# Performance work log

Hardware: AMD Instinct MI355X
Metric: run time of the kernel (lower is better)

## Reference

```python
import jax, jax.numpy as jnp
import numpy as np
from jax import lax

N = 1_000_000
H = 1024
POOL = 8
NF = 16
NS = 50
K = 5
PAD = (K - 1) // 2
D_IN = 3 + NF + NS  # 69
EPS = 1e-4


def setup_inputs() -> dict:
    key = jax.random.key(0)
    ks = jax.random.split(key, 14)
    def dense(k, fan_in, fan_out):
        lim = 1.0 / np.sqrt(fan_in)
        kw, kb = jax.random.split(k)
        w = jax.random.uniform(kw, (fan_in, fan_out), jnp.float32, -lim, lim)
        b = jax.random.uniform(kb, (fan_out,), jnp.float32, -lim, lim)
        return w, b
    x = jax.random.uniform(ks[0], (N, 2), jnp.float32)
    s = jax.random.normal(ks[1], (N, 1), jnp.float32)
    sse = jax.random.normal(ks[2], (N, NS), jnp.float32)
    sdf = jax.random.normal(ks[3], (1, 2, H, H), jnp.float32)
    lim_c = 1.0 / np.sqrt(2 * K * K)
    conv_w = jax.random.uniform(ks[4], (NF, 2, K, K), jnp.float32, -lim_c, lim_c)
    conv_b = jax.random.uniform(ks[5], (NF,), jnp.float32, -lim_c, lim_c)
    w1, b1 = dense(ks[6], D_IN, 128)
    w2, b2 = dense(ks[7], 128, 128)
    w3, b3 = dense(ks[8], 128, 96)
    w4, b4 = dense(ks[9], 96, 1)
    return {"x": x, "s": s, "sse": sse, "sdf": sdf,
            "conv_w": conv_w, "conv_b": conv_b,
            "w1": w1, "b1": b1, "w2": w2, "b2": b2,
            "w3": w3, "b3": b3, "w4": w4, "b4": b4}


def tensor_interp2d(A, pts, dx):
    # A: [C, Hh, Ww] feature map; pts: [N, 2] coords in [0,1] -> returns [N, C]
    C, Hh, Ww = A.shape
    gx = jnp.clip(pts[:, 0], dx, 1.0 - dx) * (Ww - 1)
    gy = jnp.clip(pts[:, 1], dx, 1.0 - dx) * (Hh - 1)
    x0 = jnp.floor(gx).astype(jnp.int32)
    y0 = jnp.floor(gy).astype(jnp.int32)
    x1 = jnp.minimum(x0 + 1, Ww - 1)
    y1 = jnp.minimum(y0 + 1, Hh - 1)
    wx = (gx - x0)[None, :]  # [1, N]
    wy = (gy - y0)[None, :]
    f00 = A[:, y0, x0]  # [C, N]
    f10 = A[:, y0, x1]
    f01 = A[:, y1, x0]
    f11 = A[:, y1, x1]
    out = (f00 * (1 - wx) * (1 - wy) + f10 * wx * (1 - wy)
           + f01 * (1 - wx) * wy + f11 * wx * wy)
    return out.T  # [N, C]


def reference(x, s, sse, sdf, conv_w, conv_b, w1, b1, w2, b2, w3, b3, w4, b4):
    # AvgPool2d(8, stride=8): exact reshape-mean since stride == kernel
    B, Cin, Hh, Ww = sdf.shape
    pooled = sdf.reshape(B, Cin, Hh // POOL, POOL, Ww // POOL, POOL).mean(axis=(3, 5))
    feat = lax.conv_general_dilated(pooled, conv_w, (1, 1), [(PAD, PAD), (PAD, PAD)],
                                    dimension_numbers=("NCHW", "OIHW", "NCHW"))
    feat = feat + conv_b[None, :, None, None]
    A = feat[0]  # squeeze -> [NF, 128, 128]
    x1 = tensor_interp2d(A, x, EPS)  # [N, NF]
    h = jnp.concatenate((x, s, sse, x1), axis=1)  # [N, 69]
    h = jax.nn.relu(h @ w1 + b1)
    h = jax.nn.relu(h @ w2 + b2)
    h = jax.nn.relu(h @ w3 + b3)
    return h @ w4 + b4  # [N, 1]
```

## Files before the change

kernel.cpp:

```cpp
#include <hip/hip_runtime.h>

#define EPS_ 1e-4f

typedef _Float16 f16;
typedef _Float16 f16x8 __attribute__((ext_vector_type(8)));
typedef _Float16 f16x4 __attribute__((ext_vector_type(4)));
typedef _Float16 f16x2 __attribute__((ext_vector_type(2)));
typedef __fp16 h16x2 __attribute__((ext_vector_type(2)));
typedef float f32x4v __attribute__((ext_vector_type(4)));
typedef float f32x2v __attribute__((ext_vector_type(2)));
typedef unsigned int u32;

__device__ inline f32x4v mfma16(f16x8 a, f16x8 b, f32x4v c) {
    return __builtin_amdgcn_mfma_f32_16x16x32_f16(a, b, c, 0, 0, 0);
}
__device__ inline f16x2 pk2(float a, float b) {
    h16x2 r = __builtin_amdgcn_cvt_pkrtz(a, b);
    return __builtin_bit_cast(f16x2, r);
}
__device__ inline u32 bc32(f16x2 v) { return __builtin_bit_cast(u32, v); }

__device__ inline f16x8 zero8() {
    f16x8 r;
#pragma unroll
    for (int i = 0; i < 8; i++) r[i] = (f16)0.f;
    return r;
}

__device__ inline f16x8 cvt8x2(f32x2v a, f32x2v b, f32x2v c, f32x2v d) {
    f16x2 p0 = pk2(a.x, a.y), p1 = pk2(b.x, b.y), p2 = pk2(c.x, c.y), p3 = pk2(d.x, d.y);
    f16x8 r;
    r[0] = p0[0]; r[1] = p0[1]; r[2] = p1[0]; r[3] = p1[1];
    r[4] = p2[0]; r[5] = p2[1]; r[6] = p3[0]; r[7] = p3[1];
    return r;
}

__global__ void pool_kernel(const float* __restrict__ sdf, float* __restrict__ pooled) {
    int t = blockIdx.x * blockDim.x + threadIdx.x;
    int c = t >> 14;
    int rem = t & 16383;
    int R = rem >> 7;
    int C = rem & 127;
    const float* base = sdf + c * 1048576 + (R * 8) * 1024 + C * 8;
    float sum = 0.f;
#pragma unroll
    for (int r = 0; r < 8; r++) {
        const float4* p = (const float4*)(base + r * 1024);
        float4 a = p[0];
        float4 b = p[1];
        sum += a.x + a.y + a.z + a.w + b.x + b.y + b.z + b.w;
    }
    pooled[t] = sum * (1.f / 64.f);
}

__global__ void conv_kernel(const float* __restrict__ pooled,
                            const float* __restrict__ conv_w,
                            const float* __restrict__ conv_b,
                            float* __restrict__ A) {
    int t = blockIdx.x * blockDim.x + threadIdx.x;
    int y = t >> 7, x = t & 127;
    float acc[16];
#pragma unroll
    for (int f = 0; f < 16; f++) acc[f] = conv_b[f];
#pragma unroll
    for (int c = 0; c < 2; c++) {
#pragma unroll
        for (int ky = 0; ky < 5; ky++) {
            int yy = y + ky - 2;
            if (yy < 0 || yy > 127) continue;
#pragma unroll
            for (int kx = 0; kx < 5; kx++) {
                int xx = x + kx - 2;
                if (xx < 0 || xx > 127) continue;
                float v = pooled[c * 16384 + yy * 128 + xx];
                int wbase = c * 25 + ky * 5 + kx;
#pragma unroll
                for (int f = 0; f < 16; f++)
                    acc[f] = fmaf(v, conv_w[f * 50 + wbase], acc[f]);
            }
        }
    }
    float4* out4 = (float4*)(A + t * 16);
#pragma unroll
    for (int q = 0; q < 4; q++)
        out4[q] = make_float4(acc[4 * q], acc[4 * q + 1], acc[4 * q + 2], acc[4 * q + 3]);
}

__global__ void pack_kernel(const float* __restrict__ w1, const float* __restrict__ b1,
                            const float* __restrict__ w2, const float* __restrict__ w3,
                            f16* __restrict__ frags) {
    int t = blockIdx.x * blockDim.x + threadIdx.x;
    if (t >= 80 * 64) return;
    int f = t >> 6, lane = t & 63;
    int g = lane >> 4, col = lane & 15;
    f16 v[8];
    if (f < 24) {
        int mf = f / 3, kc = f % 3;
        int o = mf * 16 + col;
#pragma unroll
        for (int i = 0; i < 8; i++) {
            int k = kc * 32 + g * 8 + i;
            float val = 0.f;
            if (k < 50) val = w1[(3 + k) * 128 + o];
            else if (k == 50) val = w1[0 * 128 + o];
            else if (k == 51) val = w1[1 * 128 + o];
            else if (k == 52) val = w1[2 * 128 + o];
            else if (k >= 56 && k < 72) val = w1[(53 + (k - 56)) * 128 + o];
            else if (k == 72) val = b1[o];
            v[i] = (f16)val;
        }
    } else if (f < 56) {
        int ff = f - 24, mf = ff >> 2, kc = ff & 3;
        int o = mf * 16 + col;
#pragma unroll
        for (int i = 0; i < 8; i++) {
            int k = kc * 32 + g * 8 + i;
            v[i] = (f16)w2[k * 128 + o];
        }
    } else {
        int ff = f - 56, mf = ff >> 2, kc = ff & 3;
        int o = mf * 16 + col;
#pragma unroll
        for (int i = 0; i < 8; i++) {
            int k = kc * 32 + g * 8 + i;
            v[i] = (f16)w3[k * 96 + o];
        }
    }
    f16* dst = frags + (f * 64 + lane) * 8;
#pragma unroll
    for (int i = 0; i < 8; i++) dst[i] = v[i];
}

__global__ void __launch_bounds__(512, 2) mlp_kernel(
    const float* __restrict__ x, const float* __restrict__ s,
    const float* __restrict__ sse, const float* __restrict__ Amat,
    const float4* __restrict__ fragsv,
    const float* __restrict__ b2, const float* __restrict__ b3,
    const float* __restrict__ w4, const float* __restrict__ b4,
    float* __restrict__ out) {
    __shared__ f16 wlds[40960];
    __shared__ f16 acth[8][2048];
    __shared__ u32 ibuf[8][2][192];
    __shared__ float bias2[128];
    __shared__ float bias3[96];
    __shared__ float w4l[96];

    const int tid = threadIdx.x;
    const int wv = tid >> 6;
    const int lane = tid & 63;
    const int g = lane >> 4, col = lane & 15;
    const int swz = (col & 7) << 3;

    {
        float4* wl4 = (float4*)wlds;
        for (int i = tid; i < 5120; i += 512) wl4[i] = fragsv[i];
        for (int i = tid; i < 128; i += 512) bias2[i] = b2[i];
        for (int i = tid; i < 96; i += 512) { bias3[i] = b3[i]; w4l[i] = w4[i]; }
    }
    __syncthreads();
    const float b4v = b4[0];

    f16* ah = acth[wv];
    u32* ibA = ibuf[wv][0];
    u32* ibB = ibuf[wv][1];

    const int wtotal = 31250;
    int wg = blockIdx.x * 8 + wv;
    const int wstride = gridDim.x * 8;

    f32x2v Ac0[4], Ac1[4], Ae, Axv; float Asv;
    f32x2v Bc0[4], Bc1[4], Be, Bxv; float Bsv;

    auto LOADT = [&](int pt0, f32x2v* c0, f32x2v* c1, f32x2v& e, f32x2v& xv, float& sv) {
        const float* base = sse + (long)(pt0 + col) * 50;
#pragma unroll
        for (int q = 0; q < 4; q++) c0[q] = *(const f32x2v*)(base + 8 * g + 2 * q);
        if (g < 2) {
#pragma unroll
            for (int q = 0; q < 4; q++) c1[q] = *(const f32x2v*)(base + 32 + 8 * g + 2 * q);
        } else if (g == 2) {
            e = *(const f32x2v*)(base + 48);
            sv = s[pt0 + col];
        }
        xv = *(const f32x2v*)(x + 2 * (pt0 + col));
    };

    auto INTERP = [&](f32x2v xv, u32* ib) {
        float gx = fminf(fmaxf(xv.x, EPS_), 1.f - EPS_) * 127.f;
        float gy = fminf(fmaxf(xv.y, EPS_), 1.f - EPS_) * 127.f;
        float fx0 = floorf(gx), fy0 = floorf(gy);
        int ix0 = (int)fx0, iy0 = (int)fy0;
        int ix1 = min(ix0 + 1, 127), iy1 = min(iy0 + 1, 127);
        float wx = gx - fx0, wy = gy - fy0;
        const f32x4v* A4 = (const f32x4v*)Amat;
        f32x4v f00 = A4[(iy0 * 128 + ix0) * 4 + g];
        f32x4v f10 = A4[(iy0 * 128 + ix1) * 4 + g];
        f32x4v f01 = A4[(iy1 * 128 + ix0) * 4 + g];
        f32x4v f11 = A4[(iy1 * 128 + ix1) * 4 + g];
        float w00 = (1.f - wx) * (1.f - wy), w10 = wx * (1.f - wy);
        float w01 = (1.f - wx) * wy, w11 = wx * wy;
        f32x4v r = f00 * w00 + f10 * w10 + f01 * w01 + f11 * w11;
        uint2 uv;
        uv.x = bc32(pk2(r.x, r.y));
        uv.y = bc32(pk2(r.z, r.w));
        *(uint2*)(ib + col * 12 + 2 * g) = uv;
    };

    auto BUILD = [&](f32x2v* c0, f32x2v* c1, f32x2v e, f32x2v xv, float sv,
                     const u32* ib, f16x8* bf) {
        bf[0] = cvt8x2(c0[0], c0[1], c0[2], c0[3]);
        if (g < 2) {
            bf[1] = cvt8x2(c1[0], c1[1], c1[2], c1[3]);
        } else if (g == 2) {
            f16x8 t = zero8();
            t[0] = (f16)e.x; t[1] = (f16)e.y;
            t[2] = (f16)xv.x; t[3] = (f16)xv.y;
            t[4] = (f16)sv;
            bf[1] = t;
        } else {
            bf[1] = *(const f16x8*)(ib + col * 12);
        }
        if (g == 0) {
            bf[2] = *(const f16x8*)(ib + col * 12 + 4);
        } else if (g == 1) {
            f16x8 t = zero8();
            t[0] = (f16)1.f;
            bf[2] = t;
        } else {
            bf[2] = zero8();
        }
    };

    auto TRANS = [&](f32x4v* acc, const float* bias, f16x8* hbf) {
#pragma unroll
        for (int mf = 0; mf < 8; mf++) {
            f32x4v v = acc[mf];
            if (bias) {
                f32x4v bb = *(const f32x4v*)&bias[mf * 16 + g * 4];
                v = v + bb;
            }
            uint2 uv;
            uv.x = bc32(pk2(fmaxf(v.x, 0.f), fmaxf(v.y, 0.f)));
            uv.y = bc32(pk2(fmaxf(v.z, 0.f), fmaxf(v.w, 0.f)));
            *(uint2*)&ah[(col * 128 + mf * 16 + g * 4) ^ swz] = uv;
        }
#pragma unroll
        for (int kc = 0; kc < 4; kc++)
            hbf[kc] = *(const f16x8*)&ah[(col * 128 + kc * 32 + g * 8) ^ swz];
    };

    auto L4OUT = [&](f32x4v* acc3, int pt0) {
        float partial = 0.f;
#pragma unroll
        for (int mf = 0; mf < 6; mf++) {
            f32x4v bb = *(const f32x4v*)&bias3[mf * 16 + g * 4];
            f32x4v wv4 = *(const f32x4v*)&w4l[mf * 16 + g * 4];
            partial += fmaxf(acc3[mf].x + bb.x, 0.f) * wv4.x;
            partial += fmaxf(acc3[mf].y + bb.y, 0.f) * wv4.y;
            partial += fmaxf(acc3[mf].z + bb.z, 0.f) * wv4.z;
            partial += fmaxf(acc3[mf].w + bb.w, 0.f) * wv4.w;
        }
        partial += __shfl_xor(partial, 16);
        partial += __shfl_xor(partial, 32);
        if (g == 0) out[pt0 + col] = partial + b4v;
    };

    if (wg < wtotal) {
        LOADT(wg * 32, Ac0, Ac1, Ae, Axv, Asv);
        LOADT(wg * 32 + 16, Bc0, Bc1, Be, Bxv, Bsv);
    }

    for (; wg < wtotal; wg += wstride) {
        const int pt0 = wg * 32;

        INTERP(Axv, ibA);
        INTERP(Bxv, ibB);

        f16x8 bfA[3], bfB[3];
        BUILD(Ac0, Ac1, Ae, Axv, Asv, ibA, bfA);
        BUILD(Bc0, Bc1, Be, Bxv, Bsv, ibB, bfB);

        int wgn = wg + wstride;
        if (wgn < wtotal) {
            LOADT(wgn * 32, Ac0, Ac1, Ae, Axv, Asv);
            LOADT(wgn * 32 + 16, Bc0, Bc1, Be, Bxv, Bsv);
        }

        f32x4v accA[8], accB[8];
#pragma unroll
        for (int mf = 0; mf < 8; mf++) {
            accA[mf] = (f32x4v)(0.f);
            accB[mf] = (f32x4v)(0.f);
        }
#pragma unroll
        for (int kc = 0; kc < 3; kc++) {
#pragma unroll
            for (int mf = 0; mf < 8; mf++) {
                f16x8 wf = *(const f16x8*)&wlds[((mf * 3 + kc) * 64 + lane) * 8];
                accA[mf] = mfma16(wf, bfA[kc], accA[mf]);
                accB[mf] = mfma16(wf, bfB[kc], accB[mf]);
            }
        }

        f16x8 hbfA[4], hbfB[4];
        TRANS(accA, nullptr, hbfA);
        TRANS(accB, nullptr, hbfB);

        f32x4v acc2A[8], acc2B[8];
#pragma unroll
        for (int mf = 0; mf < 8; mf++) {
            acc2A[mf] = (f32x4v)(0.f);
            acc2B[mf] = (f32x4v)(0.f);
        }
#pragma unroll
        for (int kc = 0; kc < 4; kc++) {
#pragma unroll
            for (int mf = 0; mf < 8; mf++) {
                f16x8 wf = *(const f16x8*)&wlds[((24 + mf * 4 + kc) * 64 + lane) * 8];
                acc2A[mf] = mfma16(wf, hbfA[kc], acc2A[mf]);
                acc2B[mf] = mfma16(wf, hbfB[kc], acc2B[mf]);
            }
        }

        TRANS(acc2A, bias2, hbfA);
        TRANS(acc2B, bias2, hbfB);

        f32x4v acc3A[6], acc3B[6];
#pragma unroll
        for (int mf = 0; mf < 6; mf++) {
            acc3A[mf] = (f32x4v)(0.f);
            acc3B[mf] = (f32x4v)(0.f);
        }
#pragma unroll
        for (int kc = 0; kc < 4; kc++) {
#pragma unroll
            for (int mf = 0; mf < 6; mf++) {
                f16x8 wf = *(const f16x8*)&wlds[((56 + mf * 4 + kc) * 64 + lane) * 8];
                acc3A[mf] = mfma16(wf, hbfA[kc], acc3A[mf]);
                acc3B[mf] = mfma16(wf, hbfB[kc], acc3B[mf]);
            }
        }

        L4OUT(acc3A, pt0);
        L4OUT(acc3B, pt0 + 16);
    }
}

extern "C" void kernel_launch(void* const* d_in, const int* in_sizes, int n_in,
                              void* d_out, int out_size, void* d_ws, size_t ws_size,
                              hipStream_t stream) {
    const float* x      = (const float*)d_in[0];
    const float* s      = (const float*)d_in[1];
    const float* sse    = (const float*)d_in[2];
    const float* sdf    = (const float*)d_in[3];
    const float* conv_w = (const float*)d_in[4];
    const float* conv_b = (const float*)d_in[5];
    const float* w1     = (const float*)d_in[6];
    const float* b1     = (const float*)d_in[7];
    const float* w2     = (const float*)d_in[8];
    const float* b2     = (const float*)d_in[9];
    const float* w3     = (const float*)d_in[10];
    const float* b3     = (const float*)d_in[11];
    const float* w4     = (const float*)d_in[12];
    const float* b4     = (const float*)d_in[13];
    float* out = (float*)d_out;

    float* pooled = (float*)d_ws;
    float* A      = pooled + 32768;
    f16*   frags  = (f16*)d_ws;

    pool_kernel<<<128, 256, 0, stream>>>(sdf, pooled);
    conv_kernel<<<64, 256, 0, stream>>>(pooled, conv_w, conv_b, A);
    pack_kernel<<<20, 256, 0, stream>>>(w1, b1, w2, w3, frags);
    mlp_kernel<<<256, 512, 0, stream>>>(x, s, sse, A, (const float4*)frags,
                                        b2, b3, w4, b4, out);
}
```

Measured before the change: 132.3 us.

## Process four 16-point tiles per wave to amortize LDS weight fragment loads

Each wave now handles 64 points per iteration (four tiles) instead of 32, so every weight fragment read from LDS feeds four MFMAs instead of two. The prefetch of the next iteration's inputs also moves from right after BUILD to after layer 3, which shortens the window it has to hide global latency. Register pressure roughly doubles (four sets of accumulators and prefetched inputs) under launch_bounds(512,2), which risks spills or lower occupancy.

```diff
diff --git a/kernel.cpp b/kernel.cpp
--- a/kernel.cpp
+++ b/kernel.cpp
@@ -140,7 +140,7 @@
     float* __restrict__ out) {
     __shared__ f16 wlds[40960];
     __shared__ f16 acth[8][2048];
-    __shared__ u32 ibuf[8][2][192];
+    __shared__ u32 ibuf[8][4][192];
     __shared__ float bias2[128];
     __shared__ float bias3[96];
     __shared__ float w4l[96];
@@ -161,33 +161,32 @@
     const float b4v = b4[0];
 
     f16* ah = acth[wv];
-    u32* ibA = ibuf[wv][0];
-    u32* ibB = ibuf[wv][1];
-
-    const int wtotal = 31250;
+
+    const int wtotal = 15625;
     int wg = blockIdx.x * 8 + wv;
     const int wstride = gridDim.x * 8;
 
-    f32x2v Ac0[4], Ac1[4], Ae, Axv; float Asv;
-    f32x2v Bc0[4], Bc1[4], Be, Bxv; float Bsv;
-
-    auto LOADT = [&](int pt0, f32x2v* c0, f32x2v* c1, f32x2v& e, f32x2v& xv, float& sv) {
+    f32x2v c0[4][4], c1[4][4], e4[4], xv4[4];
+    float sv4[4];
+
+    auto LOADT = [&](int pt0, int t) {
         const float* base = sse + (long)(pt0 + col) * 50;
 #pragma unroll
-        for (int q = 0; q < 4; q++) c0[q] = *(const f32x2v*)(base + 8 * g + 2 * q);
+        for (int q = 0; q < 4; q++) c0[t][q] = *(const f32x2v*)(base + 8 * g + 2 * q);
         if (g < 2) {
 #pragma unroll
-            for (int q = 0; q < 4; q++) c1[q] = *(const f32x2v*)(base + 32 + 8 * g + 2 * q);
+            for (int q = 0; q < 4; q++) c1[t][q] = *(const f32x2v*)(base + 32 + 8 * g + 2 * q);
         } else if (g == 2) {
-            e = *(const f32x2v*)(base + 48);
-            sv = s[pt0 + col];
-        }
-        xv = *(const f32x2v*)(x + 2 * (pt0 + col));
-    };
-
-    auto INTERP = [&](f32x2v xv, u32* ib) {
-        float gx = fminf(fmaxf(xv.x, EPS_), 1.f - EPS_) * 127.f;
-        float gy = fminf(fmaxf(xv.y, EPS_), 1.f - EPS_) * 127.f;
+            e4[t] = *(const f32x2v*)(base + 48);
+            sv4[t] = s[pt0 + col];
+        }
+        xv4[t] = *(const f32x2v*)(x + 2 * (pt0 + col));
+    };
+
+    auto INTERP = [&](int t) {
+        f32x2v xvv = xv4[t];
+        float gx = fminf(fmaxf(xvv.x, EPS_), 1.f - EPS_) * 127.f;
+        float gy = fminf(fmaxf(xvv.y, EPS_), 1.f - EPS_) * 127.f;
         float fx0 = floorf(gx), fy0 = floorf(gy);
         int ix0 = (int)fx0, iy0 = (int)fy0;
         int ix1 = min(ix0 + 1, 127), iy1 = min(iy0 + 1, 127);
@@ -203,35 +202,34 @@
         uint2 uv;
         uv.x = bc32(pk2(r.x, r.y));
         uv.y = bc32(pk2(r.z, r.w));
-        *(uint2*)(ib + col * 12 + 2 * g) = uv;
-    };
-
-    auto BUILD = [&](f32x2v* c0, f32x2v* c1, f32x2v e, f32x2v xv, float sv,
-                     const u32* ib, f16x8* bf) {
-        bf[0] = cvt8x2(c0[0], c0[1], c0[2], c0[3]);
+        *(uint2*)(&ibuf[wv][t][0] + col * 12 + 2 * g) = uv;
+    };
+
+    auto BUILD = [&](int t, f16x8* bf) {
+        bf[0] = cvt8x2(c0[t][0], c0[t][1], c0[t][2], c0[t][3]);
         if (g < 2) {
-            bf[1] = cvt8x2(c1[0], c1[1], c1[2], c1[3]);
+            bf[1] = cvt8x2(c1[t][0], c1[t][1], c1[t][2], c1[t][3]);
         } else if (g == 2) {
-            f16x8 t = zero8();
-            t[0] = (f16)e.x; t[1] = (f16)e.y;
-            t[2] = (f16)xv.x; t[3] = (f16)xv.y;
-            t[4] = (f16)sv;
-            bf[1] = t;
+            f16x8 tt = zero8();
+            tt[0] = (f16)e4[t].x; tt[1] = (f16)e4[t].y;
+            tt[2] = (f16)xv4[t].x; tt[3] = (f16)xv4[t].y;
+            tt[4] = (f16)sv4[t];
+            bf[1] = tt;
         } else {
-            bf[1] = *(const f16x8*)(ib + col * 12);
+            bf[1] = *(const f16x8*)(&ibuf[wv][t][0] + col * 12);
         }
         if (g == 0) {
-            bf[2] = *(const f16x8*)(ib + col * 12 + 4);
+            bf[2] = *(const f16x8*)(&ibuf[wv][t][0] + col * 12 + 4);
         } else if (g == 1) {
-            f16x8 t = zero8();
-            t[0] = (f16)1.f;
-            bf[2] = t;
+            f16x8 tt = zero8();
+            tt[0] = (f16)1.f;
+            bf[2] = tt;
         } else {
             bf[2] = zero8();
         }
     };
 
-    auto TRANS = [&](f32x4v* acc, const float* bias, f16x8* hbf) {
+    auto TRANS = [&](f32x4v* acc, const float* bias, f16x8* hb) {
 #pragma unroll
         for (int mf = 0; mf < 8; mf++) {
             f32x4v v = acc[mf];
@@ -246,7 +244,7 @@
         }
 #pragma unroll
         for (int kc = 0; kc < 4; kc++)
-            hbf[kc] = *(const f16x8*)&ah[(col * 128 + kc * 32 + g * 8) ^ swz];
+            hb[kc] = *(const f16x8*)&ah[(col * 128 + kc * 32 + g * 8) ^ swz];
     };
 
     auto L4OUT = [&](f32x4v* acc3, int pt0) {
@@ -266,83 +264,83 @@
     };
 
     if (wg < wtotal) {
-        LOADT(wg * 32, Ac0, Ac1, Ae, Axv, Asv);
-        LOADT(wg * 32 + 16, Bc0, Bc1, Be, Bxv, Bsv);
+#pragma unroll
+        for (int t = 0; t < 4; t++) LOADT(wg * 64 + 16 * t, t);
     }
 
     for (; wg < wtotal; wg += wstride) {
-        const int pt0 = wg * 32;
-
-        INTERP(Axv, ibA);
-        INTERP(Bxv, ibB);
-
-        f16x8 bfA[3], bfB[3];
-        BUILD(Ac0, Ac1, Ae, Axv, Asv, ibA, bfA);
-        BUILD(Bc0, Bc1, Be, Bxv, Bsv, ibB, bfB);
+        const int pt0 = wg * 64;
+
+#pragma unroll
+        for (int t = 0; t < 4; t++) INTERP(t);
+
+        f16x8 bf[4][3];
+#pragma unroll
+        for (int t = 0; t < 4; t++) BUILD(t, bf[t]);
+
+        f32x4v acc1[4][8];
+#pragma unroll
+        for (int t = 0; t < 4; t++)
+#pragma unroll
+            for (int mf = 0; mf < 8; mf++) acc1[t][mf] = (f32x4v)(0.f);
+#pragma unroll
+        for (int kc = 0; kc < 3; kc++) {
+#pragma unroll
+            for (int mf = 0; mf < 8; mf++) {
+                f16x8 wf = *(const f16x8*)&wlds[((mf * 3 + kc) * 64 + lane) * 8];
+#pragma unroll
+                for (int t = 0; t < 4; t++)
+                    acc1[t][mf] = mfma16(wf, bf[t][kc], acc1[t][mf]);
+            }
+        }
+
+        f16x8 hbf[4][4];
+#pragma unroll
+        for (int t = 0; t < 4; t++) TRANS(acc1[t], nullptr, hbf[t]);
+
+        f32x4v acc2[4][8];
+#pragma unroll
+        for (int t = 0; t < 4; t++)
+#pragma unroll
+            for (int mf = 0; mf < 8; mf++) acc2[t][mf] = (f32x4v)(0.f);
+#pragma unroll
+        for (int kc = 0; kc < 4; kc++) {
+#pragma unroll
+            for (int mf = 0; mf < 8; mf++) {
+                f16x8 wf = *(const f16x8*)&wlds[((24 + mf * 4 + kc) * 64 + lane) * 8];
+#pragma unroll
+                for (int t = 0; t < 4; t++)
+                    acc2[t][mf] = mfma16(wf, hbf[t][kc], acc2[t][mf]);
+            }
+        }
+
+#pragma unroll
+        for (int t = 0; t < 4; t++) TRANS(acc2[t], bias2, hbf[t]);
+
+        f32x4v acc3[4][6];
+#pragma unroll
+        for (int t = 0; t < 4; t++)
+#pragma unroll
+            for (int mf = 0; mf < 6; mf++) acc3[t][mf] = (f32x4v)(0.f);
+#pragma unroll
+        for (int kc = 0; kc < 4; kc++) {
+#pragma unroll
+            for (int mf = 0; mf < 6; mf++) {
+                f16x8 wf = *(const f16x8*)&wlds[((56 + mf * 4 + kc) * 64 + lane) * 8];
+#pragma unroll
+                for (int t = 0; t < 4; t++)
+                    acc3[t][mf] = mfma16(wf, hbf[t][kc], acc3[t][mf]);
+            }
+        }
 
         int wgn = wg + wstride;
         if (wgn < wtotal) {
-            LOADT(wgn * 32, Ac0, Ac1, Ae, Axv, Asv);
-            LOADT(wgn * 32 + 16, Bc0, Bc1, Be, Bxv, Bsv);
-        }
-
-        f32x4v accA[8], accB[8];
-#pragma unroll
-        for (int mf = 0; mf < 8; mf++) {
-            accA[mf] = (f32x4v)(0.f);
-            accB[mf] = (f32x4v)(0.f);
-        }
-#pragma unroll
-        for (int kc = 0; kc < 3; kc++) {
-#pragma unroll
-            for (int mf = 0; mf < 8; mf++) {
-                f16x8 wf = *(const f16x8*)&wlds[((mf * 3 + kc) * 64 + lane) * 8];
-                accA[mf] = mfma16(wf, bfA[kc], accA[mf]);
-                accB[mf] = mfma16(wf, bfB[kc], accB[mf]);
-            }
-        }
-
-        f16x8 hbfA[4], hbfB[4];
-        TRANS(accA, nullptr, hbfA);
-        TRANS(accB, nullptr, hbfB);
-
-        f32x4v acc2A[8], acc2B[8];
-#pragma unroll
-        for (int mf = 0; mf < 8; mf++) {
-            acc2A[mf] = (f32x4v)(0.f);
-            acc2B[mf] = (f32x4v)(0.f);
-        }
-#pragma unroll
-        for (int kc = 0; kc < 4; kc++) {
-#pragma unroll
-            for (int mf = 0; mf < 8; mf++) {
-                f16x8 wf = *(const f16x8*)&wlds[((24 + mf * 4 + kc) * 64 + lane) * 8];
-                acc2A[mf] = mfma16(wf, hbfA[kc], acc2A[mf]);
-                acc2B[mf] = mfma16(wf, hbfB[kc], acc2B[mf]);
-            }
-        }
-
-        TRANS(acc2A, bias2, hbfA);
-        TRANS(acc2B, bias2, hbfB);
-
-        f32x4v acc3A[6], acc3B[6];
-#pragma unroll
-        for (int mf = 0; mf < 6; mf++) {
-            acc3A[mf] = (f32x4v)(0.f);
-            acc3B[mf] = (f32x4v)(0.f);
-        }
-#pragma unroll
-        for (int kc = 0; kc < 4; kc++) {
-#pragma unroll
-            for (int mf = 0; mf < 6; mf++) {
-                f16x8 wf = *(const f16x8*)&wlds[((56 + mf * 4 + kc) * 64 + lane) * 8];
-                acc3A[mf] = mfma16(wf, hbfA[kc], acc3A[mf]);
-                acc3B[mf] = mfma16(wf, hbfB[kc], acc3B[mf]);
-            }
-        }
-
-        L4OUT(acc3A, pt0);
-        L4OUT(acc3B, pt0 + 16);
+#pragma unroll
+            for (int t = 0; t < 4; t++) LOADT(wgn * 64 + 16 * t, t);
+        }
+
+#pragma unroll
+        for (int t = 0; t < 4; t++) L4OUT(acc3[t], pt0 + 16 * t);
     }
 }
 
```

After: 268.2 us. 2.03x slower.
